# Optimization experiments

Measured on AMD Instinct MI355X. Metric: run time of the kernel, lower is better.

## Reference

```python
import jax, jax.numpy as jnp
import numpy as np

NUM_HEADS = 16


def setup_inputs() -> dict:
    key = jax.random.key(0)
    ks = jax.random.split(key, 9)
    B, N, E = 2, 2048, 1024
    s = 1.0 / np.sqrt(E).astype(np.float32)
    inp = {"x": jax.random.normal(ks[0], (B, N, E), jnp.float32)}
    names = ["q", "k", "v", "o"]
    for i, n in enumerate(names):
        inp[f"W{n}"] = jax.random.normal(ks[1 + 2 * i], (E, E), jnp.float32) * s
        inp[f"b{n}"] = jax.random.normal(ks[2 + 2 * i], (E,), jnp.float32) * 0.01
    return inp


def _feature(x):
    # act_fun = '1+elu'
    return jax.nn.elu(x) + 1.0


def reference(x, Wq, bq, Wk, bk, Wv, bv, Wo, bo):
    B, N, E = x.shape
    H = NUM_HEADS
    d = E // H

    def proj(t, W, b):  # torch nn.Linear: t @ W^T + b
        return t @ W.T + b

    def split_heads(t):  # (B,N,E) -> (B,H,N,d)
        return t.reshape(B, N, H, d).transpose(0, 2, 1, 3)

    q = _feature(split_heads(proj(x, Wq, bq)))
    k = _feature(split_heads(proj(x, Wk, bk)))
    v = split_heads(proj(x, Wv, bv))

    # causal linear attention: o_t = q_t @ cumsum_{s<=t} (k_s v_s^T)
    kv = jnp.cumsum(k[..., :, None] * v[..., None, :], axis=2)  # (B,H,N,d,d)
    o = jnp.einsum('bhnd,bhnde->bhne', q, kv)                   # (B,H,N,d)

    o = o.transpose(0, 2, 1, 3).reshape(B, N, E)
    return o @ Wo.T + bo
```

## Files before the change

kernel.cpp:

```cpp
#include <hip/hip_runtime.h>
#include <hip/hip_bf16.h>
#include <cmath>

typedef unsigned short u16;
typedef __bf16 bf16x8 __attribute__((ext_vector_type(8)));
typedef float  f32x4  __attribute__((ext_vector_type(4)));
typedef float  f4     __attribute__((ext_vector_type(4)));
typedef u16    us4    __attribute__((ext_vector_type(4)));

#define DEVFN __device__ __forceinline__

static constexpr int Bq = 2, Nq = 2048, Eq = 1024;
static constexpr int Mq = Bq * Nq;
static constexpr int CHK = 64;
static constexpr int NC  = Nq / CHK;
static constexpr int BH  = Bq * 16;

DEVFN u16 f2b(float f) {
    union { float f; unsigned int u; } x; x.f = f;
    unsigned int r = x.u + 0x7fffu + ((x.u >> 16) & 1u);
    return (u16)(r >> 16);
}

DEVFN void gl_lds16(const u16* g, u16* l) {
    __builtin_amdgcn_global_load_lds(
        (const __attribute__((address_space(1))) unsigned int*)(g),
        (__attribute__((address_space(3))) unsigned int*)(l),
        16, 0, 0);
}

DEVFN const bf16x8* frag(const u16* S, int R, int G) {
    return reinterpret_cast<const bf16x8*>(&S[R * 64 + ((G ^ (R & 7)) << 3)]);
}

__global__ __launch_bounds__(256) void cvt_kernel(const float* __restrict__ src,
                                                  u16* __restrict__ dst, int n4) {
    int i = blockIdx.x * 256 + threadIdx.x;
    if (i < n4) {
        f4 v = *reinterpret_cast<const f4*>(&src[(size_t)i * 4]);
        us4 p; p[0] = f2b(v[0]); p[1] = f2b(v[1]); p[2] = f2b(v[2]); p[3] = f2b(v[3]);
        *reinterpret_cast<us4*>(&dst[(size_t)i * 4]) = p;
    }
}

__global__ __launch_bounds__(256) void cvt4_kernel(const float* __restrict__ s0,
                                                   const float* __restrict__ s1,
                                                   const float* __restrict__ s2,
                                                   const float* __restrict__ s3,
                                                   u16* __restrict__ dst, int n4each) {
    const int which = blockIdx.y;
    const float* s = (which == 0) ? s0 : (which == 1) ? s1 : (which == 2) ? s2 : s3;
    int i = blockIdx.x * 256 + threadIdx.x;
    if (i < n4each) {
        f4 v = *reinterpret_cast<const f4*>(&s[(size_t)i * 4]);
        us4 p; p[0] = f2b(v[0]); p[1] = f2b(v[1]); p[2] = f2b(v[2]); p[3] = f2b(v[3]);
        *reinterpret_cast<us4*>(&dst[((size_t)which * n4each + i) * 4]) = p;
    }
}

template<int MODE>
__global__ __launch_bounds__(256)
void gemm_kernel(const u16* __restrict__ X, const u16* __restrict__ W,
                 const float* __restrict__ b0, const float* __restrict__ b1,
                 const float* __restrict__ b2,
                 u16* __restrict__ Qb, u16* __restrict__ Kb, u16* __restrict__ KbT,
                 u16* __restrict__ VbT, float* __restrict__ outF)
{
    constexpr int BM = (MODE == 0) ? 128 : 64;
    constexpr int MI = BM / 32;
    __shared__ u16 As[BM * 64];
    __shared__ u16 Bs[128 * 64];
    const int tid  = threadIdx.x;
    const int m0   = blockIdx.y * BM, n0 = blockIdx.x * 128;
    const int wid  = tid >> 6, lane = tid & 63;
    const int wr   = (wid >> 1) * (BM / 2), wc = (wid & 1) * 64;
    const int fr   = lane & 15, fq = lane >> 4;

    const int srow = tid >> 3;
    const int sw   = (tid & 7) ^ (srow & 7);
    const u16* gA = X + (size_t)(m0 + srow) * 1024 + sw * 8;
    const u16* gB = W + (size_t)(n0 + srow) * 1024 + sw * 8;
    u16* lA = As + wid * 512;
    u16* lB = Bs + wid * 512;

    f32x4 acc[MI][4] = {};

    for (int k0 = 0; k0 < 1024; k0 += 64) {
        __syncthreads();
#pragma unroll
        for (int i = 0; i < BM / 32; ++i)
            gl_lds16(gA + k0 + i * 32 * 1024, lA + i * 2048);
#pragma unroll
        for (int i = 0; i < 4; ++i)
            gl_lds16(gB + k0 + i * 32 * 1024, lB + i * 2048);
        __syncthreads();

#pragma unroll
        for (int kk = 0; kk < 2; ++kk) {
            bf16x8 af[MI], bfv[4];
#pragma unroll
            for (int mi = 0; mi < MI; ++mi)
                af[mi] = *frag(As, wr + mi * 16 + fr, kk * 4 + fq);
#pragma unroll
            for (int ni = 0; ni < 4; ++ni)
                bfv[ni] = *frag(Bs, wc + ni * 16 + fr, kk * 4 + fq);
#pragma unroll
            for (int mi = 0; mi < MI; ++mi)
#pragma unroll
                for (int ni = 0; ni < 4; ++ni)
                    acc[mi][ni] = __builtin_amdgcn_mfma_f32_16x16x32_bf16(
                        af[mi], bfv[ni], acc[mi][ni], 0, 0, 0);
        }
    }

    if (MODE == 0) {
        const int seg = n0 >> 10;
        const float* bp = (seg == 0) ? b0 : (seg == 1) ? b1 : b2;
#pragma unroll
        for (int mi = 0; mi < MI; ++mi)
#pragma unroll
            for (int ni = 0; ni < 4; ++ni) {
                const int nl    = (n0 & 1023) + wc + ni * 16 + fr;
                const int mbase = m0 + wr + mi * 16 + fq * 4;
                const float bn  = bp[nl];
                float vr[4];
#pragma unroll
                for (int r = 0; r < 4; ++r) {
                    float v = acc[mi][ni][r] + bn;
                    if (seg < 2) v = (v > 0.f) ? (v + 1.f) : __expf(v);
                    vr[r] = v;
                }
                if (seg == 0) {
#pragma unroll
                    for (int r = 0; r < 4; ++r)
                        Qb[(size_t)(mbase + r) * 1024 + nl] = f2b(vr[r]);
                } else {
                    us4 pk;
#pragma unroll
                    for (int r = 0; r < 4; ++r) pk[r] = f2b(vr[r]);
                    const int bb = mbase >> 11, nt = mbase & 2047;
                    const int hh = nl >> 6,     dd = nl & 63;
                    u16* T = (seg == 1) ? KbT : VbT;
                    *reinterpret_cast<us4*>(
                        &T[((size_t)(bb * 16 + hh) * 64 + dd) * 2048 + nt]) = pk;
                    if (seg == 1) {
#pragma unroll
                        for (int r = 0; r < 4; ++r)
                            Kb[(size_t)(mbase + r) * 1024 + nl] = f2b(vr[r]);
                    }
                }
            }
    } else {
#pragma unroll
        for (int mi = 0; mi < MI; ++mi)
#pragma unroll
            for (int ni = 0; ni < 4; ++ni) {
                const int n     = n0 + wc + ni * 16 + fr;
                const int mbase = m0 + wr + mi * 16 + fq * 4;
                const float bn  = b0[n];
#pragma unroll
                for (int r = 0; r < 4; ++r)
                    outF[(size_t)(mbase + r) * 1024 + n] = acc[mi][ni][r] + bn;
            }
    }
}

__global__ __launch_bounds__(64)
void chunk_kv_kernel(const u16* __restrict__ KbT, const u16* __restrict__ VbT,
                     float* __restrict__ KVT)
{
    const int blk = blockIdx.x;
    const int bh = blk >> 5, c = blk & 31;
    const int lane = threadIdx.x;
    const int fr = lane & 15, fq = lane >> 4, fk = fq * 8;
    const u16* kt = KbT + (size_t)bh * 64 * 2048;
    const u16* vt = VbT + (size_t)bh * 64 * 2048;

    bf16x8 a[4][2], b[4][2];
#pragma unroll
    for (int mi = 0; mi < 4; ++mi)
#pragma unroll
        for (int kh = 0; kh < 2; ++kh)
            a[mi][kh] = *reinterpret_cast<const bf16x8*>(
                &vt[(size_t)(mi * 16 + fr) * 2048 + c * 64 + kh * 32 + fk]);
#pragma unroll
    for (int ni = 0; ni < 4; ++ni)
#pragma unroll
        for (int kh = 0; kh < 2; ++kh)
            b[ni][kh] = *reinterpret_cast<const bf16x8*>(
                &kt[(size_t)(ni * 16 + fr) * 2048 + c * 64 + kh * 32 + fk]);

    f32x4 acc[4][4] = {};
#pragma unroll
    for (int mi = 0; mi < 4; ++mi)
#pragma unroll
        for (int ni = 0; ni < 4; ++ni)
#pragma unroll
            for (int kh = 0; kh < 2; ++kh)
                acc[mi][ni] = __builtin_amdgcn_mfma_f32_16x16x32_bf16(
                    a[mi][kh], b[ni][kh], acc[mi][ni], 0, 0, 0);

    float* out = KVT + (size_t)blk * 4096;
#pragma unroll
    for (int mi = 0; mi < 4; ++mi)
#pragma unroll
        for (int ni = 0; ni < 4; ++ni)
#pragma unroll
            for (int r = 0; r < 4; ++r)
                out[(mi * 16 + fq * 4 + r) * 64 + ni * 16 + fr] = acc[mi][ni][r];
}

__global__ __launch_bounds__(256)
void scan_kernel(const float* __restrict__ KVT, u16* __restrict__ STb)
{
    const int bh = blockIdx.x >> 4, sl = blockIdx.x & 15;
    const int el = sl * 256 + threadIdx.x;
    const float* src = KVT + (size_t)bh * NC * 4096 + el;
    u16*         dst = STb + (size_t)bh * NC * 4096 + el;
    float run = 0.f;
#pragma unroll 4
    for (int c = 0; c < NC; ++c) {
        dst[(size_t)c * 4096] = f2b(run);
        run += src[(size_t)c * 4096];
    }
}

__global__ __launch_bounds__(64)
void attn_kernel(const u16* __restrict__ Qb, const u16* __restrict__ Kb,
                 const u16* __restrict__ VbT, const u16* __restrict__ STb,
                 u16* __restrict__ Ob)
{
    __shared__ u16 P[64 * 72];
    const int blk = blockIdx.x;
    const int bh = blk >> 5, c = blk & 31;
    const int b = bh >> 4, h = bh & 15;
    const int lane = threadIdx.x;
    const int fr = lane & 15, fq = lane >> 4, fk = fq * 8;
    const int tok0 = b * 2048 + c * 64;

    bf16x8 qa[4][2];
#pragma unroll
    for (int mi = 0; mi < 4; ++mi)
#pragma unroll
        for (int kh = 0; kh < 2; ++kh)
            qa[mi][kh] = *reinterpret_cast<const bf16x8*>(
                &Qb[(size_t)(tok0 + mi * 16 + fr) * 1024 + h * 64 + kh * 32 + fk]);

    {
        bf16x8 kb[4][2];
#pragma unroll
        for (int si = 0; si < 4; ++si)
#pragma unroll
            for (int kh = 0; kh < 2; ++kh)
                kb[si][kh] = *reinterpret_cast<const bf16x8*>(
                    &Kb[(size_t)(tok0 + si * 16 + fr) * 1024 + h * 64 + kh * 32 + fk]);
        f32x4 p[4][4] = {};
#pragma unroll
        for (int mi = 0; mi < 4; ++mi)
#pragma unroll
            for (int si = 0; si < 4; ++si)
#pragma unroll
                for (int kh = 0; kh < 2; ++kh)
                    p[mi][si] = __builtin_amdgcn_mfma_f32_16x16x32_bf16(
                        qa[mi][kh], kb[si][kh], p[mi][si], 0, 0, 0);
#pragma unroll
        for (int mi = 0; mi < 4; ++mi)
#pragma unroll
            for (int si = 0; si < 4; ++si)
#pragma unroll
                for (int r = 0; r < 4; ++r) {
                    int t = mi * 16 + fq * 4 + r;
                    int s = si * 16 + fr;
                    float v = (s <= t) ? p[mi][si][r] : 0.0f;
                    P[t * 72 + s] = f2b(v);
                }
    }
    __syncthreads();

    f32x4 acc[4][4] = {};
    {
        const u16* st = STb + (size_t)blk * 4096;
        bf16x8 sb[4][2];
#pragma unroll
        for (int ni = 0; ni < 4; ++ni)
#pragma unroll
            for (int kh = 0; kh < 2; ++kh)
                sb[ni][kh] = *reinterpret_cast<const bf16x8*>(
                    &st[(ni * 16 + fr) * 64 + kh * 32 + fk]);
#pragma unroll
        for (int mi = 0; mi < 4; ++mi)
#pragma unroll
            for (int ni = 0; ni < 4; ++ni)
#pragma unroll
                for (int kh = 0; kh < 2; ++kh)
                    acc[mi][ni] = __builtin_amdgcn_mfma_f32_16x16x32_bf16(
                        qa[mi][kh], sb[ni][kh], acc[mi][ni], 0, 0, 0);
    }
    {
        const u16* vt = VbT + (size_t)bh * 64 * 2048;
#pragma unroll
        for (int sh = 0; sh < 2; ++sh) {
            bf16x8 pa[4], vb[4];
#pragma unroll
            for (int mi = 0; mi < 4; ++mi)
                pa[mi] = *reinterpret_cast<const bf16x8*>(
                    &P[(mi * 16 + fr) * 72 + sh * 32 + fk]);
#pragma unroll
            for (int ni = 0; ni < 4; ++ni)
                vb[ni] = *reinterpret_cast<const bf16x8*>(
                    &vt[(size_t)(ni * 16 + fr) * 2048 + c * 64 + sh * 32 + fk]);
#pragma unroll
            for (int mi = 0; mi < 4; ++mi)
#pragma unroll
                for (int ni = 0; ni < 4; ++ni)
                    acc[mi][ni] = __builtin_amdgcn_mfma_f32_16x16x32_bf16(
                        pa[mi], vb[ni], acc[mi][ni], 0, 0, 0);
        }
    }
#pragma unroll
    for (int mi = 0; mi < 4; ++mi)
#pragma unroll
        for (int ni = 0; ni < 4; ++ni)
#pragma unroll
            for (int r = 0; r < 4; ++r) {
                int t = tok0 + mi * 16 + fq * 4 + r;
                int n = h * 64 + ni * 16 + fr;
                Ob[(size_t)t * 1024 + n] = f2b(acc[mi][ni][r]);
            }
}

extern "C" void kernel_launch(void* const* d_in, const int* in_sizes, int n_in,
                              void* d_out, int out_size, void* d_ws, size_t ws_size,
                              hipStream_t stream)
{
    (void)in_sizes; (void)n_in; (void)out_size; (void)ws_size;
    const float* x  = (const float*)d_in[0];
    const float* Wq = (const float*)d_in[1];
    const float* bq = (const float*)d_in[2];
    const float* Wk = (const float*)d_in[3];
    const float* bk = (const float*)d_in[4];
    const float* Wv = (const float*)d_in[5];
    const float* bv = (const float*)d_in[6];
    const float* Wo = (const float*)d_in[7];
    const float* bo = (const float*)d_in[8];
    float* out = (float*)d_out;

    char* ws = (char*)d_ws;
    constexpr size_t SZ_ME = (size_t)Mq * Eq * 2;
    u16*   Qb  = (u16*)  (ws + 0 * SZ_ME);
    u16*   Kb  = (u16*)  (ws + 1 * SZ_ME);
    u16*   KbT = (u16*)  (ws + 2 * SZ_ME);
    u16*   VbT = (u16*)  (ws + 3 * SZ_ME);
    u16*   Ob  = (u16*)  (ws + 4 * SZ_ME);
    float* KVT = (float*)(ws + 5 * SZ_ME);
    u16*   STb = (u16*)  (ws + 5 * SZ_ME + (size_t)BH * NC * 4096 * 4);
    u16*   Xb  = (u16*)  (ws + 6 * SZ_ME + (size_t)BH * NC * 4096 * 4);
    u16*   Wb0 = (u16*)  (ws + 7 * SZ_ME + (size_t)BH * NC * 4096 * 4);
    u16* Wqkvb = Wb0;
    u16* Wob   = Wb0 + (size_t)3 * Eq * Eq;

    {
        int n4x = Mq * Eq / 4;
        cvt_kernel<<<dim3((n4x + 255) / 256), dim3(256), 0, stream>>>(x, Xb, n4x);
        int n4w = Eq * Eq / 4;
        cvt4_kernel<<<dim3((n4w + 255) / 256, 4), dim3(256), 0, stream>>>(
            Wq, Wk, Wv, Wo, Wb0, n4w);
    }

    gemm_kernel<0><<<dim3(24, 32), dim3(256), 0, stream>>>(
        Xb, Wqkvb, bq, bk, bv, Qb, Kb, KbT, VbT, nullptr);

    chunk_kv_kernel<<<dim3(BH * NC), dim3(64), 0, stream>>>(KbT, VbT, KVT);
    scan_kernel<<<dim3(BH * 16), dim3(256), 0, stream>>>(KVT, STb);
    attn_kernel<<<dim3(BH * NC), dim3(64), 0, stream>>>(Qb, Kb, VbT, STb, Ob);

    gemm_kernel<1><<<dim3(8, 64), dim3(256), 0, stream>>>(
        Ob, Wob, bo, nullptr, nullptr, nullptr, nullptr, nullptr, nullptr, out);
}
```

Before: 102.9 us.

## Rewrite QKV projection GEMM with 256x256 tiles and 4-stage LDS pipeline

Replaces the templated QKV GEMM with a dedicated kernel that uses 512-thread blocks, 256x256 output tiles and a K-step of 32. It keeps a 4-buffer LDS ring filled by direct global-to-LDS loads two steps ahead, with split barriers and setprio around the MFMA phases. The aim is more data reuse per block and better overlap of memory loads with matrix math. The cost is heavy register use (8x4 accumulators), only 192 blocks across the device, and large LDS use. The output projection moves unchanged into its own kernel.

```diff
diff --git a/kernel.cpp b/kernel.cpp
--- a/kernel.cpp
+++ b/kernel.cpp
@@ -27,10 +27,6 @@
         (const __attribute__((address_space(1))) unsigned int*)(g),
         (__attribute__((address_space(3))) unsigned int*)(l),
         16, 0, 0);
-}
-
-DEVFN const bf16x8* frag(const u16* S, int R, int G) {
-    return reinterpret_cast<const bf16x8*>(&S[R * 64 + ((G ^ (R & 7)) << 3)]);
 }
 
 __global__ __launch_bounds__(256) void cvt_kernel(const float* __restrict__ src,
@@ -58,15 +54,141 @@
     }
 }
 
-template<int MODE>
+__global__ __launch_bounds__(512, 2)
+void qkv_kernel(const u16* __restrict__ X, const u16* __restrict__ W,
+                const float* __restrict__ b0, const float* __restrict__ b1,
+                const float* __restrict__ b2,
+                u16* __restrict__ Qb, u16* __restrict__ Kb, u16* __restrict__ KbT,
+                u16* __restrict__ VbT)
+{
+    __shared__ u16 lds[4 * 16384];
+    const int tid  = threadIdx.x;
+    const int m0   = blockIdx.y * 256, n0 = blockIdx.x * 256;
+    const int wid  = tid >> 6, lane = tid & 63;
+    const int wr   = (wid >> 2) * 128;
+    const int wc   = (wid & 3) * 64;
+    const int fr   = lane & 15, fq = lane >> 4;
+
+    const int srow  = tid >> 2;
+    const int scol8 = ((tid & 3) ^ (srow & 3)) * 8;
+    const u16* gX = X + (size_t)(m0 + srow) * 1024 + scol8;
+    const u16* gW = W + (size_t)(n0 + srow) * 1024 + scol8;
+    const int dbase = srow * 32 + (tid & 3) * 8;
+
+    const int fsw = ((fq ^ (fr & 3)) << 3);
+    int aoff[2][4], boff[4];
+#pragma unroll
+    for (int mh = 0; mh < 2; ++mh)
+#pragma unroll
+        for (int mi = 0; mi < 4; ++mi)
+            aoff[mh][mi] = (wr + mh * 64 + mi * 16 + fr) * 32 + fsw;
+#pragma unroll
+    for (int ni = 0; ni < 4; ++ni)
+        boff[ni] = 8192 + (wc + ni * 16 + fr) * 32 + fsw;
+
+#define STAGE(kt, r) do {                                                          \
+        const u16* _s = (((r) >> 1) ? gW : gX) + (size_t)((r)&1) * 131072 + (kt) * 32; \
+        u16* _d = lds + ((kt)&3) * 16384 + ((r) >> 1) * 8192 + ((r)&1) * 4096 + dbase; \
+        gl_lds16(_s, _d);                                                          \
+    } while (0)
+
+#pragma unroll
+    for (int r = 0; r < 4; ++r) STAGE(0, r);
+#pragma unroll
+    for (int r = 0; r < 4; ++r) STAGE(1, r);
+    asm volatile("s_waitcnt vmcnt(4)" ::: "memory");
+    __builtin_amdgcn_sched_barrier(0);
+    __builtin_amdgcn_s_barrier();
+
+    f32x4 acc[8][4] = {};
+
+    for (int t = 0; t < 32; ++t) {
+        const u16* buf = lds + (t & 3) * 16384;
+        bf16x8 a[4], b[4];
+#pragma unroll
+        for (int ni = 0; ni < 4; ++ni)
+            b[ni] = *reinterpret_cast<const bf16x8*>(&buf[boff[ni]]);
+#pragma unroll
+        for (int mi = 0; mi < 4; ++mi)
+            a[mi] = *reinterpret_cast<const bf16x8*>(&buf[aoff[0][mi]]);
+        if (t + 2 < 32) { STAGE(t + 2, 0); STAGE(t + 2, 1); }
+        __builtin_amdgcn_s_barrier();
+        __builtin_amdgcn_s_setprio(1);
+#pragma unroll
+        for (int mi = 0; mi < 4; ++mi)
+#pragma unroll
+            for (int ni = 0; ni < 4; ++ni)
+                acc[mi][ni] = __builtin_amdgcn_mfma_f32_16x16x32_bf16(
+                    a[mi], b[ni], acc[mi][ni], 0, 0, 0);
+        __builtin_amdgcn_s_setprio(0);
+        __builtin_amdgcn_s_barrier();
+#pragma unroll
+        for (int mi = 0; mi < 4; ++mi)
+            a[mi] = *reinterpret_cast<const bf16x8*>(&buf[aoff[1][mi]]);
+        if (t + 2 < 32) { STAGE(t + 2, 2); STAGE(t + 2, 3); }
+        __builtin_amdgcn_s_barrier();
+        __builtin_amdgcn_s_setprio(1);
+#pragma unroll
+        for (int mi = 0; mi < 4; ++mi)
+#pragma unroll
+            for (int ni = 0; ni < 4; ++ni)
+                acc[4 + mi][ni] = __builtin_amdgcn_mfma_f32_16x16x32_bf16(
+                    a[mi], b[ni], acc[4 + mi][ni], 0, 0, 0);
+        __builtin_amdgcn_s_setprio(0);
+        if (t < 30)       asm volatile("s_waitcnt vmcnt(4)" ::: "memory");
+        else if (t == 30) asm volatile("s_waitcnt vmcnt(0)" ::: "memory");
+        __builtin_amdgcn_sched_barrier(0);
+        __builtin_amdgcn_s_barrier();
+    }
+#undef STAGE
+
+    const int seg = n0 >> 10;
+    const float* bp = (seg == 0) ? b0 : (seg == 1) ? b1 : b2;
+#pragma unroll
+    for (int mg = 0; mg < 8; ++mg)
+#pragma unroll
+        for (int ni = 0; ni < 4; ++ni) {
+            const int nl    = (n0 & 1023) + wc + ni * 16 + fr;
+            const int mbase = m0 + wr + mg * 16 + fq * 4;
+            const float bn  = bp[nl];
+            float vr[4];
+#pragma unroll
+            for (int r = 0; r < 4; ++r) {
+                float v = acc[mg][ni][r] + bn;
+                if (seg < 2) v = (v > 0.f) ? (v + 1.f) : __expf(v);
+                vr[r] = v;
+            }
+            if (seg == 0) {
+#pragma unroll
+                for (int r = 0; r < 4; ++r)
+                    Qb[(size_t)(mbase + r) * 1024 + nl] = f2b(vr[r]);
+            } else {
+                us4 pk;
+#pragma unroll
+                for (int r = 0; r < 4; ++r) pk[r] = f2b(vr[r]);
+                const int bb = mbase >> 11, nt = mbase & 2047;
+                const int hh = nl >> 6,     dd = nl & 63;
+                u16* T = (seg == 1) ? KbT : VbT;
+                *reinterpret_cast<us4*>(
+                    &T[((size_t)(bb * 16 + hh) * 64 + dd) * 2048 + nt]) = pk;
+                if (seg == 1) {
+#pragma unroll
+                    for (int r = 0; r < 4; ++r)
+                        Kb[(size_t)(mbase + r) * 1024 + nl] = f2b(vr[r]);
+                }
+            }
+        }
+}
+
+DEVFN const bf16x8* frag(const u16* S, int R, int G) {
+    return reinterpret_cast<const bf16x8*>(&S[R * 64 + ((G ^ (R & 7)) << 3)]);
+}
+
 __global__ __launch_bounds__(256)
-void gemm_kernel(const u16* __restrict__ X, const u16* __restrict__ W,
-                 const float* __restrict__ b0, const float* __restrict__ b1,
-                 const float* __restrict__ b2,
-                 u16* __restrict__ Qb, u16* __restrict__ Kb, u16* __restrict__ KbT,
-                 u16* __restrict__ VbT, float* __restrict__ outF)
-{
-    constexpr int BM = (MODE == 0) ? 128 : 64;
+void oproj_kernel(const u16* __restrict__ X, const u16* __restrict__ W,
+                  const float* __restrict__ b0, float* __restrict__ outF)
+{
+    constexpr int BM = 64;
     constexpr int MI = BM / 32;
     __shared__ u16 As[BM * 64];
     __shared__ u16 Bs[128 * 64];
@@ -113,56 +235,17 @@
         }
     }
 
-    if (MODE == 0) {
-        const int seg = n0 >> 10;
-        const float* bp = (seg == 0) ? b0 : (seg == 1) ? b1 : b2;
-#pragma unroll
-        for (int mi = 0; mi < MI; ++mi)
-#pragma unroll
-            for (int ni = 0; ni < 4; ++ni) {
-                const int nl    = (n0 & 1023) + wc + ni * 16 + fr;
-                const int mbase = m0 + wr + mi * 16 + fq * 4;
-                const float bn  = bp[nl];
-                float vr[4];
-#pragma unroll
-                for (int r = 0; r < 4; ++r) {
-                    float v = acc[mi][ni][r] + bn;
-                    if (seg < 2) v = (v > 0.f) ? (v + 1.f) : __expf(v);
-                    vr[r] = v;
-                }
-                if (seg == 0) {
-#pragma unroll
-                    for (int r = 0; r < 4; ++r)
-                        Qb[(size_t)(mbase + r) * 1024 + nl] = f2b(vr[r]);
-                } else {
-                    us4 pk;
-#pragma unroll
-                    for (int r = 0; r < 4; ++r) pk[r] = f2b(vr[r]);
-                    const int bb = mbase >> 11, nt = mbase & 2047;
-                    const int hh = nl >> 6,     dd = nl & 63;
-                    u16* T = (seg == 1) ? KbT : VbT;
-                    *reinterpret_cast<us4*>(
-                        &T[((size_t)(bb * 16 + hh) * 64 + dd) * 2048 + nt]) = pk;
-                    if (seg == 1) {
-#pragma unroll
-                        for (int r = 0; r < 4; ++r)
-                            Kb[(size_t)(mbase + r) * 1024 + nl] = f2b(vr[r]);
-                    }
-                }
-            }
-    } else {
-#pragma unroll
-        for (int mi = 0; mi < MI; ++mi)
-#pragma unroll
-            for (int ni = 0; ni < 4; ++ni) {
-                const int n     = n0 + wc + ni * 16 + fr;
-                const int mbase = m0 + wr + mi * 16 + fq * 4;
-                const float bn  = b0[n];
-#pragma unroll
-                for (int r = 0; r < 4; ++r)
-                    outF[(size_t)(mbase + r) * 1024 + n] = acc[mi][ni][r] + bn;
-            }
-    }
+#pragma unroll
+    for (int mi = 0; mi < MI; ++mi)
+#pragma unroll
+        for (int ni = 0; ni < 4; ++ni) {
+            const int n     = n0 + wc + ni * 16 + fr;
+            const int mbase = m0 + wr + mi * 16 + fq * 4;
+            const float bn  = b0[n];
+#pragma unroll
+            for (int r = 0; r < 4; ++r)
+                outF[(size_t)(mbase + r) * 1024 + n] = acc[mi][ni][r] + bn;
+        }
 }
 
 __global__ __launch_bounds__(64)
@@ -367,13 +450,12 @@
             Wq, Wk, Wv, Wo, Wb0, n4w);
     }
 
-    gemm_kernel<0><<<dim3(24, 32), dim3(256), 0, stream>>>(
-        Xb, Wqkvb, bq, bk, bv, Qb, Kb, KbT, VbT, nullptr);
+    qkv_kernel<<<dim3(12, 16), dim3(512), 0, stream>>>(
+        Xb, Wqkvb, bq, bk, bv, Qb, Kb, KbT, VbT);
 
     chunk_kv_kernel<<<dim3(BH * NC), dim3(64), 0, stream>>>(KbT, VbT, KVT);
     scan_kernel<<<dim3(BH * 16), dim3(256), 0, stream>>>(KVT, STb);
     attn_kernel<<<dim3(BH * NC), dim3(64), 0, stream>>>(Qb, Kb, VbT, STb, Ob);
 
-    gemm_kernel<1><<<dim3(8, 64), dim3(256), 0, stream>>>(
-        Ob, Wob, bo, nullptr, nullptr, nullptr, nullptr, nullptr, nullptr, out);
-}
+    oproj_kernel<<<dim3(8, 64), dim3(256), 0, stream>>>(Ob, Wob, bo, out);
+}
```

Result: no change. 103.5 us (+0.5%).
